# Kernel optimization log

Hardware: AMD Instinct MI355X
Metric: run time of the kernel (lower is better)

## Reference

```python
import jax, jax.numpy as jnp
import numpy as np

B, S, H, R, IN, OPS, NPAD = 128, 128, 512, 16, 2, 5, 16
L = IN + NPAD
NEG = -1e12


def setup_inputs():
    key = jax.random.key(0)
    ks = jax.random.split(key, 32)
    def n(k, shape, scale=1.0):
        return jax.random.normal(k, shape, jnp.float32) * scale
    s = 0.05
    return {
        "encoder_outputs": n(ks[0], (S, B, H)),
        "current_emb": n(ks[1], (B, 1, H)),
        "left_childs": n(ks[2], (B, H)),
        "padding_hidden": jnp.zeros((1, H), jnp.float32),
        "num_pades": n(ks[3], (B, NPAD, H)),
        "rule_scores": n(ks[4], (R, H)),
        "embedding_weight": n(ks[5], (1, IN, H)),
        "W_concat_l": n(ks[6], (H, H), s), "b_concat_l": jnp.zeros((H,)),
        "W_concat_lg": n(ks[7], (H, H), s), "b_concat_lg": jnp.zeros((H,)),
        "W_concat_r": n(ks[8], (2 * H, H), s), "b_concat_r": jnp.zeros((H,)),
        "W_concat_rg": n(ks[9], (2 * H, H), s), "b_concat_rg": jnp.zeros((H,)),
        "W_tree_attn": n(ks[10], (2 * H, H), s), "b_tree_attn": jnp.zeros((H,)),
        "W_tree_score": n(ks[11], (H, 1), s), "b_tree_score": jnp.zeros((1,)),
        "W_rule_attn": n(ks[12], (2 * H, H), s), "b_rule_attn": jnp.zeros((H,)),
        "W_rule_score": n(ks[13], (H, 1), s), "b_rule_score": jnp.zeros((1,)),
        "W_rp1": n(ks[14], (H, H), s), "b_rp1": jnp.zeros((H,)),
        "W_rp2": n(ks[15], (H, 1), s), "b_rp2": jnp.zeros((1,)),
        "W_sc_attn": n(ks[16], (3 * H, H), s), "b_sc_attn": jnp.zeros((H,)),
        "W_sc_score": n(ks[17], (H, 1), s),
        "W_ops": n(ks[18], (2 * H, OPS), s), "b_ops": jnp.zeros((OPS,)),
        "seq_mask": jax.random.randint(ks[19], (B, S), 0, 2).astype(jnp.int32),
        "mask_nums": jax.random.randint(ks[20], (B, L), 0, 2).astype(jnp.int32),
        "has_left": jax.random.randint(ks[21], (B,), 0, 2).astype(jnp.int32),
        "stack_empty": jax.random.randint(ks[22], (B,), 0, 2).astype(jnp.int32),
    }


def reference(encoder_outputs, current_emb, left_childs, padding_hidden, num_pades,
              rule_scores, embedding_weight,
              W_concat_l, b_concat_l, W_concat_lg, b_concat_lg,
              W_concat_r, b_concat_r, W_concat_rg, b_concat_rg,
              W_tree_attn, b_tree_attn, W_tree_score, b_tree_score,
              W_rule_attn, b_rule_attn, W_rule_score, b_rule_score,
              W_rp1, b_rp1, W_rp2, b_rp2,
              W_sc_attn, b_sc_attn, W_sc_score, W_ops, b_ops,
              seq_mask, mask_nums, has_left, stack_empty):
    sm = seq_mask.astype(bool)          # [B,S] True = pad
    nm = mask_nums.astype(bool)         # [B,L]
    hl = has_left.astype(bool)[:, None]
    se = stack_empty.astype(bool)[:, None]
    h = encoder_outputs.shape[-1]
    # gather top-of-stack embedding, padding for empty stacks (the ragged python loop)
    c = jnp.where(se, padding_hidden[0], current_emb[:, 0])  # [B,H]
    # gated combine: left_child==None branch vs cat(left, c) branch (dropout=eval)
    node_l = jnp.tanh(c @ W_concat_l + b_concat_l) * jax.nn.sigmoid(c @ W_concat_lg + b_concat_lg)
    node_r = (jnp.tanh(left_childs @ W_concat_r[:h] + c @ W_concat_r[h:] + b_concat_r)
              * jax.nn.sigmoid(left_childs @ W_concat_rg[:h] + c @ W_concat_rg[h:] + b_concat_rg))
    q = jnp.where(hl, node_r, node_l)                        # [B,H]
    current_node = q[:, None, :]                              # [B,1,H]
    # TreeAttn: concat(hidden, enc) -> Linear -> tanh -> Linear(H,1) -> softmax over S
    e = jnp.tanh(q @ W_tree_attn[:h] + encoder_outputs @ W_tree_attn[h:] + b_tree_attn)  # [S,B,H]
    ae = (e @ W_tree_score)[..., 0] + b_tree_score[0]         # [S,B]
    ae = jnp.where(sm, NEG, ae.T)                             # [B,S]
    current_attn = jax.nn.softmax(ae, axis=1)                 # [B,S]
    current_context = jnp.einsum('bs,sbh->bh', current_attn, encoder_outputs)[:, None, :]
    # RuleAttn: concat(enc, rule) additive attention, softmax over S
    re = jnp.tanh(encoder_outputs @ W_rule_attn[:h]
                  + (rule_scores @ W_rule_attn[h:])[:, None, None, :]
                  + b_rule_attn)                              # [R,S,B,H]
    r_ae = (re @ W_rule_score)[..., 0] + b_rule_score[0]      # [R,S,B]
    r_ae = jnp.transpose(r_ae, (2, 0, 1))                     # [B,R,S]
    r_ae = jnp.where(sm[:, None, :], NEG, r_ae)
    rules_attn = jax.nn.softmax(r_ae, axis=-1)
    rules_context = jnp.einsum('brs,sbh->brh', rules_attn + 0.2 * current_attn[:, None, :], encoder_outputs)
    rule_prob = jax.nn.softmax((jnp.tanh(rules_context @ W_rp1 + b_rp1) @ W_rp2)[..., 0] + b_rp2[0], axis=-1)  # [B,R]
    # leaf scoring: Score(cat(node, context), [const_embs | num_pades])
    bsz = q.shape[0]
    ew = jnp.concatenate([jnp.broadcast_to(embedding_weight, (bsz,) + embedding_weight.shape[1:]), num_pades], axis=1)  # [B,L,H]
    leaf = jnp.concatenate([q, current_context[:, 0]], axis=1)  # [B,2H]
    sc = jnp.tanh((leaf @ W_sc_attn[:2 * h])[:, None, :] + ew @ W_sc_attn[2 * h:] + b_sc_attn)  # [B,L,H]
    num_score = jnp.where(nm, NEG, (sc @ W_sc_score)[..., 0])   # [B,L]
    op = leaf @ W_ops + b_ops                                   # [B,OPS]
    return num_score, op, current_node, current_context, ew, rule_prob
```

## Files before the change

### kernel.cpp

```cpp
#include <hip/hip_runtime.h>
#include <hip/hip_bf16.h>

#define B_ 128
#define S_ 128
#define H_ 512
#define R_ 16
#define IN_ 2
#define OPS_ 5
#define NPAD_ 16
#define L_ 18
#define NEGV (-1000000000000.0f)
#define C2_ (-2.885390081777927f)

typedef __bf16 bf16_t;
typedef bf16_t bf16x8 __attribute__((ext_vector_type(8)));
typedef float floatx4 __attribute__((ext_vector_type(4)));

__device__ __forceinline__ float rcp_f(float x) { return __builtin_amdgcn_rcpf(x); }
__device__ __forceinline__ float exp2_f(float x) { return __builtin_amdgcn_exp2f(x); }

__device__ __forceinline__ float fast_tanh(float x) {
    return 2.0f * rcp_f(1.0f + exp2_f(C2_ * x)) - 1.0f;
}
__device__ __forceinline__ float fast_sigmoid(float x) {
    return rcp_f(1.0f + exp2_f(-1.4426950408889634f * x));
}
__device__ __forceinline__ unsigned short f2bf(float f) {
    unsigned int u = __builtin_bit_cast(unsigned int, f);
    u += 0x7fff + ((u >> 16) & 1);
    return (unsigned short)(u >> 16);
}
__device__ __forceinline__ float bf2f(unsigned short u) {
    return __builtin_bit_cast(float, (unsigned int)u << 16);
}

#define LSTR 40

__device__ __forceinline__ void mfma_tile(const unsigned short* __restrict__ A,
                                          const unsigned short* __restrict__ Bt,
                                          void* __restrict__ Cv, bool bf16_out,
                                          int m0, int n0, int K, int ldc,
                                          unsigned short* As, unsigned short* Bs) {
    const int tid  = threadIdx.x;
    const int wid  = tid >> 6, lane = tid & 63;
    const int quad = lane >> 4, mn = lane & 15;
    const int wm = (wid & 1) * 64, wn = (wid >> 1) * 64;
    const int sr = tid >> 2;
    const int sc = (tid & 3) * 8;

    const unsigned short* pa0 = A  + (size_t)(m0 + sr)      * K + sc;
    const unsigned short* pa1 = A  + (size_t)(m0 + sr + 64) * K + sc;
    const unsigned short* pb0 = Bt + (size_t)(n0 + sr)      * K + sc;
    const unsigned short* pb1 = Bt + (size_t)(n0 + sr + 64) * K + sc;

    uint4 a0 = *(const uint4*)pa0;
    uint4 a1 = *(const uint4*)pa1;
    uint4 b0 = *(const uint4*)pb0;
    uint4 b1 = *(const uint4*)pb1;

    floatx4 acc[4][4] = {};

    for (int k0 = 0; k0 < K; k0 += 32) {
        __syncthreads();
        *(uint4*)&As[sr * LSTR + sc]        = a0;
        *(uint4*)&As[(sr + 64) * LSTR + sc] = a1;
        *(uint4*)&Bs[sr * LSTR + sc]        = b0;
        *(uint4*)&Bs[(sr + 64) * LSTR + sc] = b1;
        __syncthreads();

        if (k0 + 32 < K) {
            a0 = *(const uint4*)(pa0 + k0 + 32);
            a1 = *(const uint4*)(pa1 + k0 + 32);
            b0 = *(const uint4*)(pb0 + k0 + 32);
            b1 = *(const uint4*)(pb1 + k0 + 32);
        }

        bf16x8 af[4], bfr[4];
        #pragma unroll
        for (int i = 0; i < 4; ++i)
            af[i] = *(const bf16x8*)&As[(wm + i * 16 + mn) * LSTR + quad * 8];
        #pragma unroll
        for (int j = 0; j < 4; ++j)
            bfr[j] = *(const bf16x8*)&Bs[(wn + j * 16 + mn) * LSTR + quad * 8];

        #pragma unroll
        for (int i = 0; i < 4; ++i)
            #pragma unroll
            for (int j = 0; j < 4; ++j)
                acc[i][j] = __builtin_amdgcn_mfma_f32_16x16x32_bf16(af[i], bfr[j], acc[i][j], 0, 0, 0);
    }

    #pragma unroll
    for (int i = 0; i < 4; ++i) {
        #pragma unroll
        for (int j = 0; j < 4; ++j) {
            #pragma unroll
            for (int r = 0; r < 4; ++r) {
                int row = m0 + wm + i * 16 + quad * 4 + r;
                int col = n0 + wn + j * 16 + mn;
                if (bf16_out)
                    ((unsigned short*)Cv)[(size_t)row * ldc + col] = f2bf(acc[i][j][r]);
                else
                    ((float*)Cv)[(size_t)row * ldc + col] = acc[i][j][r];
            }
        }
    }
}

__global__ __launch_bounds__(256) void k_gemm_mega1(const unsigned short* __restrict__ EO_bf,
                                                    const unsigned short* __restrict__ Wcat,
                                                    unsigned short* __restrict__ eobuf,
                                                    const unsigned short* __restrict__ q_bf,
                                                    const unsigned short* __restrict__ T5,
                                                    float* __restrict__ qT) {
    __shared__ unsigned short As[128 * LSTR];
    __shared__ unsigned short Bs[128 * LSTR];
    int blk = blockIdx.x;
    if (blk < 1024)
        mfma_tile(EO_bf, Wcat, eobuf, true, (blk & 127) * 128, (blk >> 7) * 128, 512, 1024, As, Bs);
    else
        mfma_tile(q_bf, T5, qT, false, 0, (blk - 1024) * 128, 512, 512, As, Bs);
}

__global__ __launch_bounds__(256) void k_gemm_mega2(const unsigned short* __restrict__ rctx_bf,
                                                    const unsigned short* __restrict__ T8,
                                                    float* __restrict__ rclin,
                                                    const unsigned short* __restrict__ leaf_bf,
                                                    const unsigned short* __restrict__ T9,
                                                    float* __restrict__ lsb,
                                                    const unsigned short* __restrict__ ew_bf,
                                                    const unsigned short* __restrict__ T10,
                                                    unsigned short* __restrict__ ewp_bf) {
    __shared__ unsigned short As[128 * LSTR];
    __shared__ unsigned short Bs[128 * LSTR];
    int blk = blockIdx.x;
    if (blk < 64)
        mfma_tile(rctx_bf, T8, rclin, false, (blk >> 2) * 128, (blk & 3) * 128, 512, 512, As, Bs);
    else if (blk < 68)
        mfma_tile(leaf_bf, T9, lsb, false, 0, (blk - 64) * 128, 1024, 512, As, Bs);
    else {
        int r = blk - 68;
        mfma_tile(ew_bf, T10, ewp_bf, true, (r >> 2) * 128, (r & 3) * 128, 512, 512, As, Bs);
    }
}

struct MJ5 {
    const unsigned short* A[5]; const unsigned short* Bt[5]; float* C[5];
    int M[5]; int K[5];
};
__global__ __launch_bounds__(256) void gemm_bf16_j5(MJ5 g) {
    __shared__ unsigned short As[128 * LSTR];
    __shared__ unsigned short Bs[128 * LSTR];

    const int z = blockIdx.z;
    const unsigned short* A  = g.A[z];
    const unsigned short* Bt = g.Bt[z];
    float* C = g.C[z];
    const int M = g.M[z], K = g.K[z];

    const int tid  = threadIdx.x;
    const int wid  = tid >> 6, lane = tid & 63;
    const int quad = lane >> 4, mn = lane & 15;
    const int wm = (wid & 1) * 64, wn = (wid >> 1) * 64;
    const int n0 = blockIdx.x * 128;

    const int sr = tid >> 2;
    const int sc = (tid & 3) * 8;
    const int ra0 = min(sr, M - 1);
    const int ra1 = min(sr + 64, M - 1);

    const unsigned short* pa0 = A  + (size_t)ra0 * K + sc;
    const unsigned short* pa1 = A  + (size_t)ra1 * K + sc;
    const unsigned short* pb0 = Bt + (size_t)(n0 + sr)      * K + sc;
    const unsigned short* pb1 = Bt + (size_t)(n0 + sr + 64) * K + sc;

    uint4 a0 = *(const uint4*)pa0;
    uint4 a1 = *(const uint4*)pa1;
    uint4 b0 = *(const uint4*)pb0;
    uint4 b1 = *(const uint4*)pb1;

    floatx4 acc[4][4] = {};

    for (int k0 = 0; k0 < K; k0 += 32) {
        __syncthreads();
        *(uint4*)&As[sr * LSTR + sc]        = a0;
        *(uint4*)&As[(sr + 64) * LSTR + sc] = a1;
        *(uint4*)&Bs[sr * LSTR + sc]        = b0;
        *(uint4*)&Bs[(sr + 64) * LSTR + sc] = b1;
        __syncthreads();

        if (k0 + 32 < K) {
            a0 = *(const uint4*)(pa0 + k0 + 32);
            a1 = *(const uint4*)(pa1 + k0 + 32);
            b0 = *(const uint4*)(pb0 + k0 + 32);
            b1 = *(const uint4*)(pb1 + k0 + 32);
        }

        bf16x8 af[4], bfr[4];
        #pragma unroll
        for (int i = 0; i < 4; ++i)
            af[i] = *(const bf16x8*)&As[(wm + i * 16 + mn) * LSTR + quad * 8];
        #pragma unroll
        for (int j = 0; j < 4; ++j)
            bfr[j] = *(const bf16x8*)&Bs[(wn + j * 16 + mn) * LSTR + quad * 8];

        #pragma unroll
        for (int i = 0; i < 4; ++i)
            #pragma unroll
            for (int j = 0; j < 4; ++j)
                acc[i][j] = __builtin_amdgcn_mfma_f32_16x16x32_bf16(af[i], bfr[j], acc[i][j], 0, 0, 0);
    }

    #pragma unroll
    for (int i = 0; i < 4; ++i) {
        #pragma unroll
        for (int j = 0; j < 4; ++j) {
            #pragma unroll
            for (int r = 0; r < 4; ++r) {
                int row = wm + i * 16 + quad * 4 + r;
                int col = n0 + wn + j * 16 + mn;
                if (row < M)
                    C[(size_t)row * 512 + col] = acc[i][j][r];
            }
        }
    }
}

struct PrepArgs {
    const float *EO, *cur, *padh, *left, *rsc, *embw, *npad;
    const int* se;
    unsigned short *EO_bf, *c_bf, *acat_bf, *rsc_bf, *ew_bf;
    float* ew_out;
    const float* tsrc[11];
    unsigned short* tdst[11];
    int tK[11];
    int tbase[12];
};
#define PG_CAST 8192
#define PG_EW   1152
#define PG_PREP 288
#define PG_WT   3584
#define PG_TOTAL (PG_CAST + PG_EW + PG_PREP + PG_WT)

__global__ __launch_bounds__(256) void k_prep_mega(PrepArgs a) {
    __shared__ float t[32][33];
    int blk = blockIdx.x, tid = threadIdx.x;
    if (blk < PG_CAST) {
        int i = (blk * 256 + tid) * 4;
        float4 v = *(const float4*)(a.EO + i);
        ushort4 o;
        o.x = f2bf(v.x); o.y = f2bf(v.y); o.z = f2bf(v.z); o.w = f2bf(v.w);
        *(ushort4*)(a.EO_bf + i) = o;
    } else if (blk < PG_CAST + PG_EW) {
        int i = ((blk - PG_CAST) * 256 + tid) * 4;
        int j = i & 511;
        int bl = i >> 9;
        int l = bl % L_;
        int b = bl / L_;
        const float* src = (l < IN_) ? (a.embw + l * H_ + j)
                                     : (a.npad + ((size_t)b * NPAD_ + (l - IN_)) * H_ + j);
        float4 v = *(const float4*)src;
        *(float4*)(a.ew_out + i) = v;
        ushort4 o;
        o.x = f2bf(v.x); o.y = f2bf(v.y); o.z = f2bf(v.z); o.w = f2bf(v.w);
        *(ushort4*)(a.ew_bf + i) = o;
    } else if (blk < PG_CAST + PG_EW + PG_PREP) {
        int i = (blk - PG_CAST - PG_EW) * 256 + tid;
        if (i < B_ * H_) {
            int b = i >> 9, j = i & 511;
            float cv = a.se[b] ? a.padh[j] : a.cur[i];
            a.c_bf[i] = f2bf(cv);
            a.acat_bf[b * 1024 + j] = f2bf(a.left[i]);
            a.acat_bf[b * 1024 + 512 + j] = f2bf(cv);
        } else {
            int k = i - B_ * H_;
            a.rsc_bf[k] = f2bf(a.rsc[k]);
        }
    } else {
        int rel = blk - (PG_CAST + PG_EW + PG_PREP);
        int j = 0;
        while (rel >= a.tbase[j + 1]) ++j;
        int r = rel - a.tbase[j];
        int K = a.tK[j];
        const float* src = a.tsrc[j];
        unsigned short* dst = a.tdst[j];
        int bx = (r & 15) * 32;
        int by = (r >> 4) * 32;
        int tx = tid & 31, ty = tid >> 5;
        #pragma unroll
        for (int i = 0; i < 32; i += 8)
            t[ty + i][tx] = src[(size_t)(by + ty + i) * 512 + bx + tx];
        __syncthreads();
        #pragma unroll
        for (int i = 0; i < 32; i += 8)
            dst[(size_t)(bx + ty + i) * K + by + tx] = f2bf(t[tx][ty + i]);
    }
}

__global__ void k_node(const float* __restrict__ gl, const float* __restrict__ glg,
                       const float* __restrict__ gr, const float* __restrict__ grg,
                       const float* __restrict__ bl, const float* __restrict__ blg,
                       const float* __restrict__ br, const float* __restrict__ brg,
                       const int* __restrict__ hl,
                       unsigned short* __restrict__ q_bf, float* __restrict__ node_out,
                       unsigned short* __restrict__ leaf_bf) {
    int i = blockIdx.x * blockDim.x + threadIdx.x;
    int b = i >> 9, j = i & 511;
    float nl = fast_tanh(gl[i] + bl[j]) * fast_sigmoid(glg[i] + blg[j]);
    float nr = fast_tanh(gr[i] + br[j]) * fast_sigmoid(grg[i] + brg[j]);
    float v = hl[b] ? nr : nl;
    node_out[i] = v;
    q_bf[i] = f2bf(v);
    leaf_bf[b * 1024 + j] = f2bf(v);
}

__global__ __launch_bounds__(256) void k_score_fused(const float* __restrict__ qT,
                                                     const unsigned short* __restrict__ eobuf,
                                                     const float* __restrict__ b_ta,
                                                     const float* __restrict__ w_ts,
                                                     const float* __restrict__ b_ts,
                                                     const float* __restrict__ RP,
                                                     const float* __restrict__ b_ra,
                                                     const float* __restrict__ w_rs,
                                                     const float* __restrict__ b_rs,
                                                     const int* __restrict__ sm,
                                                     float* __restrict__ attn,
                                                     float* __restrict__ comb) {
    __shared__ float sc[S_];
    int blk = blockIdx.x;
    int tid = threadIdx.x;
    int wid = tid >> 6, lane = tid & 63;
    int j0 = lane * 8;

    if (blk < 128) {
        int b = blk;
        float4 q0 = *(const float4*)(qT + b * H_ + j0);
        float4 q1 = *(const float4*)(qT + b * H_ + j0 + 4);
        float4 t0 = *(const float4*)(b_ta + j0);
        float4 t1 = *(const float4*)(b_ta + j0 + 4);
        float4 w0 = *(const float4*)(w_ts + j0);
        float4 w1 = *(const float4*)(w_ts + j0 + 4);
        float qc[8] = {C2_*(q0.x+t0.x), C2_*(q0.y+t0.y), C2_*(q0.z+t0.z), C2_*(q0.w+t0.w),
                       C2_*(q1.x+t1.x), C2_*(q1.y+t1.y), C2_*(q1.z+t1.z), C2_*(q1.w+t1.w)};
        float w2[8] = {2*w0.x, 2*w0.y, 2*w0.z, 2*w0.w, 2*w1.x, 2*w1.y, 2*w1.z, 2*w1.w};
        float wsum = 0.5f * (w2[0]+w2[1]+w2[2]+w2[3]+w2[4]+w2[5]+w2[6]+w2[7]);
        float bias = b_ts[0];

        for (int s = wid; s < S_; s += 4) {
            if (sm[b * S_ + s]) {
                if (lane == 0) sc[s] = NEGV;
                continue;
            }
            uint4 ev = *(const uint4*)(eobuf + ((size_t)s * B_ + b) * 1024 + j0);
            const unsigned short* ep = (const unsigned short*)&ev;
            float acc = -wsum;
            #pragma unroll
            for (int k = 0; k < 8; ++k) {
                float y = fmaf(C2_, bf2f(ep[k]), qc[k]);
                acc = fmaf(w2[k], rcp_f(1.0f + exp2_f(y)), acc);
            }
            #pragma unroll
            for (int o = 32; o > 0; o >>= 1) acc += __shfl_xor(acc, o);
            if (lane == 0) sc[s] = acc + bias;
        }
        __syncthreads();
        if (tid < 64) {
            float v0 = sc[tid], v1 = sc[tid + 64];
            float m = fmaxf(v0, v1);
            #pragma unroll
            for (int o = 32; o > 0; o >>= 1) m = fmaxf(m, __shfl_xor(m, o));
            float e0 = __expf(v0 - m), e1 = __expf(v1 - m);
            float ss = e0 + e1;
            #pragma unroll
            for (int o = 32; o > 0; o >>= 1) ss += __shfl_xor(ss, o);
            float r = rcp_f(ss);
            attn[b * S_ + tid] = e0 * r;
            attn[b * S_ + tid + 64] = e1 * r;
        }
        return;
    }

    int row = (blk - 128) * 4 + wid;
    int s = row >> 7, b = row & 127;
    bool masked = sm[b * S_ + s] != 0;
    if (masked) {
        if (lane < R_) comb[((size_t)b * R_ + lane) * S_ + s] = NEGV;
        return;
    }
    uint4 ev = *(const uint4*)(eobuf + (size_t)row * 1024 + 512 + j0);
    const unsigned short* ep = (const unsigned short*)&ev;
    float4 a0 = *(const float4*)(b_ra + j0);
    float4 a1 = *(const float4*)(b_ra + j0 + 4);
    float4 w0 = *(const float4*)(w_rs + j0);
    float4 w1 = *(const float4*)(w_rs + j0 + 4);
    float ba[8] = {a0.x, a0.y, a0.z, a0.w, a1.x, a1.y, a1.z, a1.w};
    float w2[8], ed[8];
    float wsum = 0.f;
    {
        float w[8] = {w0.x, w0.y, w0.z, w0.w, w1.x, w1.y, w1.z, w1.w};
        #pragma unroll
        for (int k = 0; k < 8; ++k) {
            wsum += w[k];
            w2[k] = 2.0f * w[k];
            ed[k] = C2_ * (bf2f(ep[k]) + ba[k]);
        }
    }
    float bias = b_rs[0];
    #pragma unroll
    for (int r = 0; r < R_; ++r) {
        float4 r0 = *(const float4*)(RP + r * H_ + j0);
        float4 r1 = *(const float4*)(RP + r * H_ + j0 + 4);
        float rp[8] = {r0.x, r0.y, r0.z, r0.w, r1.x, r1.y, r1.z, r1.w};
        float acc = -wsum;
        #pragma unroll
        for (int k = 0; k < 8; ++k) {
            float y = fmaf(C2_, rp[k], ed[k]);
            acc = fmaf(w2[k], rcp_f(1.0f + exp2_f(y)), acc);
        }
        #pragma unroll
        for (int o = 32; o > 0; o >>= 1) acc += __shfl_xor(acc, o);
        if (lane == 0) comb[((size_t)b * R_ + r) * S_ + s] = acc + bias;
    }
}

__global__ __launch_bounds__(512) void k_ctxsm(const unsigned short* __restrict__ EO_bf,
                                               const float* __restrict__ attn,
                                               const float* __restrict__ comb,
                                               const int* __restrict__ sm,
                                               float* __restrict__ ctx_out,
                                               unsigned short* __restrict__ leaf_bf,
                                               unsigned short* __restrict__ rctx) {
    __shared__ float cb[R_ * S_];
    __shared__ float at[S_];
    __shared__ int smr[S_];
    int b = blockIdx.x;
    int tid = threadIdx.x;
    int w = tid >> 6, lane = tid & 63;

    if (tid < S_) {
        at[tid] = attn[b * S_ + tid];
        smr[tid] = sm[b * S_ + tid];
    }
    for (int i = tid; i < R_ * S_; i += 512) cb[i] = comb[(size_t)b * R_ * S_ + i];
    __syncthreads();

    #pragma unroll
    for (int rr = 0; rr < 2; ++rr) {
        int r = w * 2 + rr;
        float v0 = cb[r * S_ + lane], v1 = cb[r * S_ + lane + 64];
        float m = fmaxf(v0, v1);
        #pragma unroll
        for (int o = 32; o > 0; o >>= 1) m = fmaxf(m, __shfl_xor(m, o));
        float e0 = __expf(v0 - m), e1 = __expf(v1 - m);
        float ss = e0 + e1;
        #pragma unroll
        for (int o = 32; o > 0; o >>= 1) ss += __shfl_xor(ss, o);
        float rc_ = rcp_f(ss);
        cb[r * S_ + lane]      = e0 * rc_ + 0.2f * at[lane];
        cb[r * S_ + lane + 64] = e1 * rc_ + 0.2f * at[lane + 64];
    }
    __syncthreads();

    int j = tid;
    float ctx = 0.f;
    float rc[R_] = {};
    for (int s = 0; s < S_; ++s) {
        if (smr[s]) continue;
        float eo = bf2f(EO_bf[((size_t)s * B_ + b) * H_ + j]);
        ctx += at[s] * eo;
        #pragma unroll
        for (int r = 0; r < R_; ++r) rc[r] += cb[r * S_ + s] * eo;
    }
    ctx_out[b * H_ + j] = ctx;
    leaf_bf[b * 1024 + 512 + j] = f2bf(ctx);
    #pragma unroll
    for (int r = 0; r < R_; ++r) rctx[((size_t)b * R_ + r) * H_ + j] = f2bf(rc[r]);
}

__global__ __launch_bounds__(256) void k_epilogue(const float* __restrict__ rclin,
                                                  const float* __restrict__ b_rp1,
                                                  const float* __restrict__ w_rp2,
                                                  const float* __restrict__ b_rp2,
                                                  float* __restrict__ prob,
                                                  const float* __restrict__ lsb,
                                                  const unsigned short* __restrict__ ewp,
                                                  const float* __restrict__ b_sc,
                                                  const float* __restrict__ w_scs,
                                                  const int* __restrict__ mask_nums,
                                                  float* __restrict__ ns_out,
                                                  const unsigned short* __restrict__ leaf_bf,
                                                  const float* __restrict__ Wops,
                                                  const float* __restrict__ bops,
                                                  float* __restrict__ op_out) {
    __shared__ float sc[R_];
    int blk = blockIdx.x;
    int wid = threadIdx.x >> 6, lane = threadIdx.x & 63;
    if (blk < 128) {
        int b = blk;
        int j0 = lane * 8;
        float4 p0 = *(const float4*)(b_rp1 + j0);
        float4 p1 = *(const float4*)(b_rp1 + j0 + 4);
        float4 w0 = *(const float4*)(w_rp2 + j0);
        float4 w1 = *(const float4*)(w_rp2 + j0 + 4);
        float brc[8] = {C2_*p0.x, C2_*p0.y, C2_*p0.z, C2_*p0.w,
                        C2_*p1.x, C2_*p1.y, C2_*p1.z, C2_*p1.w};
        float w[8] = {w0.x, w0.y, w0.z, w0.w, w1.x, w1.y, w1.z, w1.w};
        float wsum = 0.f;
        #pragma unroll
        for (int k = 0; k < 8; ++k) wsum += w[k];
        #pragma unroll
        for (int rr = 0; rr < 4; ++rr) {
            int r = wid * 4 + rr;
            const float* rl = rclin + ((size_t)b * R_ + r) * H_ + j0;
            float4 r0 = *(const float4*)(rl);
            float4 r1 = *(const float4*)(rl + 4);
            float rv[8] = {r0.x, r0.y, r0.z, r0.w, r1.x, r1.y, r1.z, r1.w};
            float acc = -wsum;
            #pragma unroll
            for (int k = 0; k < 8; ++k) {
                float y = fmaf(C2_, rv[k], brc[k]);
                acc = fmaf(2.0f * w[k], rcp_f(1.0f + exp2_f(y)), acc);
            }
            #pragma unroll
            for (int o = 32; o > 0; o >>= 1) acc += __shfl_xor(acc, o);
            if (lane == 0) sc[r] = acc + b_rp2[0];
        }
        __syncthreads();
        if (threadIdx.x < R_) {
            float m = -1e30f;
            for (int r = 0; r < R_; ++r) m = fmaxf(m, sc[r]);
            float sum = 0.f;
            for (int r = 0; r < R_; ++r) sum += __expf(sc[r] - m);
            prob[b * R_ + threadIdx.x] = __expf(sc[threadIdx.x] - m) * rcp_f(sum);
        }
    } else if (blk < 704) {
        int row = (blk - 128) * 4 + wid;
        int b = row / L_, l = row - b * L_;
        bool masked = mask_nums[b * L_ + l] != 0;
        if (masked) {
            if (lane == 0) ns_out[b * L_ + l] = NEGV;
            return;
        }
        int j0 = lane * 8;
        uint4 ev = *(const uint4*)(ewp + (size_t)row * H_ + j0);
        const unsigned short* ep = (const unsigned short*)&ev;
        float4 l0 = *(const float4*)(lsb + b * H_ + j0);
        float4 l1 = *(const float4*)(lsb + b * H_ + j0 + 4);
        float4 s0 = *(const float4*)(b_sc + j0);
        float4 s1 = *(const float4*)(b_sc + j0 + 4);
        float4 w0 = *(const float4*)(w_scs + j0);
        float4 w1 = *(const float4*)(w_scs + j0 + 4);
        float lc[8] = {C2_*(l0.x+s0.x), C2_*(l0.y+s0.y), C2_*(l0.z+s0.z), C2_*(l0.w+s0.w),
                       C2_*(l1.x+s1.x), C2_*(l1.y+s1.y), C2_*(l1.z+s1.z), C2_*(l1.w+s1.w)};
        float w[8] = {w0.x, w0.y, w0.z, w0.w, w1.x, w1.y, w1.z, w1.w};
        float wsum = 0.f;
        #pragma unroll
        for (int k = 0; k < 8; ++k) wsum += w[k];
        float acc = -wsum;
        #pragma unroll
        for (int k = 0; k < 8; ++k) {
            float y = fmaf(C2_, bf2f(ep[k]), lc[k]);
            acc = fmaf(2.0f * w[k], rcp_f(1.0f + exp2_f(y)), acc);
        }
        #pragma unroll
        for (int o = 32; o > 0; o >>= 1) acc += __shfl_xor(acc, o);
        if (lane == 0) ns_out[b * L_ + l] = acc;
    } else {
        int b = (blk - 704) * 4 + wid;
        int base = b * 1024 + lane * 16;
        uint4 v0 = *(const uint4*)(leaf_bf + base);
        uint4 v1 = *(const uint4*)(leaf_bf + base + 8);
        const unsigned short* lp0 = (const unsigned short*)&v0;
        const unsigned short* lp1 = (const unsigned short*)&v1;
        float lv[16];
        #pragma unroll
        for (int k = 0; k < 8; ++k) { lv[k] = bf2f(lp0[k]); lv[8 + k] = bf2f(lp1[k]); }
        #pragma unroll
        for (int o = 0; o < OPS_; ++o) {
            float acc = 0.f;
            #pragma unroll
            for (int k = 0; k < 16; ++k)
                acc = fmaf(lv[k], Wops[(size_t)(lane * 16 + k) * OPS_ + o], acc);
            #pragma unroll
            for (int of = 32; of > 0; of >>= 1) acc += __shfl_xor(acc, of);
            if (lane == 0) op_out[b * OPS_ + o] = acc + bops[o];
        }
    }
}

extern "C" void kernel_launch(void* const* d_in, const int* in_sizes, int n_in,
                              void* d_out, int out_size, void* d_ws, size_t ws_size,
                              hipStream_t stream) {
    const float* EO   = (const float*)d_in[0];
    const float* cur  = (const float*)d_in[1];
    const float* left = (const float*)d_in[2];
    const float* padh = (const float*)d_in[3];
    const float* npad = (const float*)d_in[4];
    const float* rsc  = (const float*)d_in[5];
    const float* embw = (const float*)d_in[6];
    const float* Wl   = (const float*)d_in[7];  const float* bl   = (const float*)d_in[8];
    const float* Wlg  = (const float*)d_in[9];  const float* blg  = (const float*)d_in[10];
    const float* Wr   = (const float*)d_in[11]; const float* br   = (const float*)d_in[12];
    const float* Wrg  = (const float*)d_in[13]; const float* brg  = (const float*)d_in[14];
    const float* Wta  = (const float*)d_in[15]; const float* bta  = (const float*)d_in[16];
    const float* Wts  = (const float*)d_in[17]; const float* bts  = (const float*)d_in[18];
    const float* Wra  = (const float*)d_in[19]; const float* bra  = (const float*)d_in[20];
    const float* Wrs  = (const float*)d_in[21]; const float* brs  = (const float*)d_in[22];
    const float* Wrp1 = (const float*)d_in[23]; const float* brp1 = (const float*)d_in[24];
    const float* Wrp2 = (const float*)d_in[25]; const float* brp2 = (const float*)d_in[26];
    const float* Wsa  = (const float*)d_in[27]; const float* bsa  = (const float*)d_in[28];
    const float* Wss  = (const float*)d_in[29];
    const float* Wops = (const float*)d_in[30]; const float* bops = (const float*)d_in[31];
    const int* smk = (const int*)d_in[32];
    const int* nmk = (const int*)d_in[33];
    const int* hlk = (const int*)d_in[34];
    const int* sek = (const int*)d_in[35];

    float* out = (float*)d_out;

    const size_t O_NS    = 0;
    const size_t O_OP    = O_NS + (size_t)B_ * L_;
    const size_t O_NODE  = O_OP + (size_t)B_ * OPS_;
    const size_t O_CTX   = O_NODE + (size_t)B_ * H_;
    const size_t O_EW    = O_CTX + (size_t)B_ * H_;
    const size_t O_RPROB = O_EW + (size_t)B_ * L_ * H_;

    float* f = (float*)d_ws;
    float* rp_buf = f;               f += 8192;
    float* qT     = f;               f += 65536;
    float* attn   = f;               f += 16384;
    float* comb   = f;               f += 262144;
    float* gl     = f;               f += 65536;
    float* glg    = f;               f += 65536;
    float* gr     = f;               f += 65536;
    float* grg    = f;               f += 65536;
    float* lsb    = f;               f += 65536;
    float* rclin  = f;               f += 1048576;
    unsigned short* u = (unsigned short*)f;
    unsigned short* EO_bf   = u;     u += 8388608;
    unsigned short* ew_bf   = u;     u += 1179648;
    unsigned short* leaf_bf = u;     u += 131072;
    unsigned short* rctx_bf = u;     u += 1048576;
    unsigned short* Wcat    = u;     u += 524288;
    unsigned short* T0      = u;     u += 262144;
    unsigned short* T1      = u;     u += 262144;
    unsigned short* T2      = u;     u += 524288;
    unsigned short* T3      = u;     u += 524288;
    unsigned short* T4      = u;     u += 262144;
    unsigned short* T5      = u;     u += 262144;
    unsigned short* T8      = u;     u += 262144;
    unsigned short* T9      = u;     u += 524288;
    unsigned short* T10     = u;     u += 262144;
    unsigned short* q_bf    = u;     u += 65536;
    unsigned short* c_bf    = u;     u += 65536;
    unsigned short* acat_bf = u;     u += 131072;
    unsigned short* rsc_bf  = u;     u += 8192;
    unsigned short* ewp_bf  = u;     u += 1179648;
    unsigned short* eobuf   = u;     u += 16777216;

    PrepArgs a;
    a.EO = EO; a.cur = cur; a.padh = padh; a.left = left; a.rsc = rsc;
    a.embw = embw; a.npad = npad; a.se = sek;
    a.EO_bf = EO_bf; a.c_bf = c_bf; a.acat_bf = acat_bf; a.rsc_bf = rsc_bf;
    a.ew_bf = ew_bf; a.ew_out = out + O_EW;
    const float* tsrc[11] = {Wl, Wlg, Wr, Wrg, Wra + (size_t)H_ * H_, Wta,
                             Wta + (size_t)H_ * H_, Wra, Wrp1, Wsa, Wsa + (size_t)2 * H_ * H_};
    unsigned short* tdst[11] = {T0, T1, T2, T3, T4, T5, Wcat, Wcat + 512 * 512, T8, T9, T10};
    int tk[11] = {512, 512, 1024, 1024, 512, 512, 512, 512, 512, 1024, 512};
    int base = 0;
    for (int i = 0; i < 11; ++i) {
        a.tsrc[i] = tsrc[i]; a.tdst[i] = tdst[i]; a.tK[i] = tk[i];
        a.tbase[i] = base;
        base += 16 * (tk[i] / 32);
    }
    a.tbase[11] = base;
    k_prep_mega<<<PG_TOTAL, 256, 0, stream>>>(a);

    MJ5 g;
    g.A[0] = c_bf;    g.Bt[0] = T0; g.C[0] = gl;     g.M[0] = B_;  g.K[0] = 512;
    g.A[1] = c_bf;    g.Bt[1] = T1; g.C[1] = glg;    g.M[1] = B_;  g.K[1] = 512;
    g.A[2] = acat_bf; g.Bt[2] = T2; g.C[2] = gr;     g.M[2] = B_;  g.K[2] = 1024;
    g.A[3] = acat_bf; g.Bt[3] = T3; g.C[3] = grg;    g.M[3] = B_;  g.K[3] = 1024;
    g.A[4] = rsc_bf;  g.Bt[4] = T4; g.C[4] = rp_buf; g.M[4] = R_;  g.K[4] = 512;
    gemm_bf16_j5<<<dim3(4, 1, 5), 256, 0, stream>>>(g);

    k_node<<<256, 256, 0, stream>>>(gl, glg, gr, grg, bl, blg, br, brg, hlk,
                                    q_bf, out + O_NODE, leaf_bf);

    k_gemm_mega1<<<1028, 256, 0, stream>>>(EO_bf, Wcat, eobuf, q_bf, T5, qT);

    k_score_fused<<<128 + S_ * B_ / 4, 256, 0, stream>>>(
        qT, eobuf, bta, Wts, bts, rp_buf, bra, Wrs, brs, smk, attn, comb);

    k_ctxsm<<<B_, 512, 0, stream>>>(EO_bf, attn, comb, smk, out + O_CTX,
                                    leaf_bf, rctx_bf);

    k_gemm_mega2<<<140, 256, 0, stream>>>(rctx_bf, T8, rclin, leaf_bf, T9, lsb,
                                          ew_bf, T10, ewp_bf);

    k_epilogue<<<736, 256, 0, stream>>>(rclin, brp1, Wrp2, brp2, out + O_RPROB,
                                        lsb, ewp_bf, bsa, Wss, nmk, out + O_NS,
                                        leaf_bf, Wops, bops, out + O_OP);
}
```

Before: 298.2 us.

## Double-buffer GEMM LDS tiles, vectorize epilogue stores, split ctx kernel over H

The shared GEMM tile routines now use two LDS buffers, so the next K-slice is written while MFMAs consume the current one, cutting one barrier per iteration. MFMA operands are swapped so each lane holds four consecutive output columns, which lets the epilogue write float4/ushort4 vectors instead of scalar stores. The context kernel is split into two 256-thread blocks per batch row along H and walks a compacted list of unmasked positions instead of branching on the mask. This doubles LDS per GEMM block, which may lower occupancy, and builds the position list serially in one thread.

```diff
diff --git a/kernel.cpp b/kernel.cpp
--- a/kernel.cpp
+++ b/kernel.cpp
@@ -35,6 +35,7 @@
 }
 
 #define LSTR 40
+#define LBUF (128 * LSTR)
 
 __device__ __forceinline__ void mfma_tile(const unsigned short* __restrict__ A,
                                           const unsigned short* __restrict__ Bt,
@@ -57,51 +58,69 @@
     uint4 a1 = *(const uint4*)pa1;
     uint4 b0 = *(const uint4*)pb0;
     uint4 b1 = *(const uint4*)pb1;
+    *(uint4*)&As[sr * LSTR + sc]        = a0;
+    *(uint4*)&As[(sr + 64) * LSTR + sc] = a1;
+    *(uint4*)&Bs[sr * LSTR + sc]        = b0;
+    *(uint4*)&Bs[(sr + 64) * LSTR + sc] = b1;
+    if (K > 32) {
+        a0 = *(const uint4*)(pa0 + 32);
+        a1 = *(const uint4*)(pa1 + 32);
+        b0 = *(const uint4*)(pb0 + 32);
+        b1 = *(const uint4*)(pb1 + 32);
+    }
+    __syncthreads();
 
     floatx4 acc[4][4] = {};
 
     for (int k0 = 0; k0 < K; k0 += 32) {
-        __syncthreads();
-        *(uint4*)&As[sr * LSTR + sc]        = a0;
-        *(uint4*)&As[(sr + 64) * LSTR + sc] = a1;
-        *(uint4*)&Bs[sr * LSTR + sc]        = b0;
-        *(uint4*)&Bs[(sr + 64) * LSTR + sc] = b1;
-        __syncthreads();
+        const int cur = (k0 >> 5) & 1;
+        unsigned short* Asb = As + cur * LBUF;
+        unsigned short* Bsb = Bs + cur * LBUF;
+
+        bf16x8 af[4], bfr[4];
+        #pragma unroll
+        for (int i = 0; i < 4; ++i)
+            af[i] = *(const bf16x8*)&Asb[(wm + i * 16 + mn) * LSTR + quad * 8];
+        #pragma unroll
+        for (int j = 0; j < 4; ++j)
+            bfr[j] = *(const bf16x8*)&Bsb[(wn + j * 16 + mn) * LSTR + quad * 8];
+
+        #pragma unroll
+        for (int i = 0; i < 4; ++i)
+            #pragma unroll
+            for (int j = 0; j < 4; ++j)
+                acc[i][j] = __builtin_amdgcn_mfma_f32_16x16x32_bf16(bfr[j], af[i], acc[i][j], 0, 0, 0);
 
         if (k0 + 32 < K) {
-            a0 = *(const uint4*)(pa0 + k0 + 32);
-            a1 = *(const uint4*)(pa1 + k0 + 32);
-            b0 = *(const uint4*)(pb0 + k0 + 32);
-            b1 = *(const uint4*)(pb1 + k0 + 32);
-        }
-
-        bf16x8 af[4], bfr[4];
-        #pragma unroll
-        for (int i = 0; i < 4; ++i)
-            af[i] = *(const bf16x8*)&As[(wm + i * 16 + mn) * LSTR + quad * 8];
-        #pragma unroll
-        for (int j = 0; j < 4; ++j)
-            bfr[j] = *(const bf16x8*)&Bs[(wn + j * 16 + mn) * LSTR + quad * 8];
-
-        #pragma unroll
-        for (int i = 0; i < 4; ++i)
-            #pragma unroll
-            for (int j = 0; j < 4; ++j)
-                acc[i][j] = __builtin_amdgcn_mfma_f32_16x16x32_bf16(af[i], bfr[j], acc[i][j], 0, 0, 0);
+            unsigned short* Asn = As + (cur ^ 1) * LBUF;
+            unsigned short* Bsn = Bs + (cur ^ 1) * LBUF;
+            *(uint4*)&Asn[sr * LSTR + sc]        = a0;
+            *(uint4*)&Asn[(sr + 64) * LSTR + sc] = a1;
+            *(uint4*)&Bsn[sr * LSTR + sc]        = b0;
+            *(uint4*)&Bsn[(sr + 64) * LSTR + sc] = b1;
+            if (k0 + 64 < K) {
+                a0 = *(const uint4*)(pa0 + k0 + 64);
+                a1 = *(const uint4*)(pa1 + k0 + 64);
+                b0 = *(const uint4*)(pb0 + k0 + 64);
+                b1 = *(const uint4*)(pb1 + k0 + 64);
+            }
+            __syncthreads();
+        }
     }
 
     #pragma unroll
     for (int i = 0; i < 4; ++i) {
+        int row = m0 + wm + i * 16 + mn;
         #pragma unroll
         for (int j = 0; j < 4; ++j) {
-            #pragma unroll
-            for (int r = 0; r < 4; ++r) {
-                int row = m0 + wm + i * 16 + quad * 4 + r;
-                int col = n0 + wn + j * 16 + mn;
-                if (bf16_out)
-                    ((unsigned short*)Cv)[(size_t)row * ldc + col] = f2bf(acc[i][j][r]);
-                else
-                    ((float*)Cv)[(size_t)row * ldc + col] = acc[i][j][r];
+            int col = n0 + wn + j * 16 + quad * 4;
+            if (bf16_out) {
+                ushort4 v = {f2bf(acc[i][j][0]), f2bf(acc[i][j][1]),
+                             f2bf(acc[i][j][2]), f2bf(acc[i][j][3])};
+                *(ushort4*)((unsigned short*)Cv + (size_t)row * ldc + col) = v;
+            } else {
+                float4 v = {acc[i][j][0], acc[i][j][1], acc[i][j][2], acc[i][j][3]};
+                *(float4*)((float*)Cv + (size_t)row * ldc + col) = v;
             }
         }
     }
@@ -113,8 +132,8 @@
                                                     const unsigned short* __restrict__ q_bf,
                                                     const unsigned short* __restrict__ T5,
                                                     float* __restrict__ qT) {
-    __shared__ unsigned short As[128 * LSTR];
-    __shared__ unsigned short Bs[128 * LSTR];
+    __shared__ unsigned short As[2 * LBUF];
+    __shared__ unsigned short Bs[2 * LBUF];
     int blk = blockIdx.x;
     if (blk < 1024)
         mfma_tile(EO_bf, Wcat, eobuf, true, (blk & 127) * 128, (blk >> 7) * 128, 512, 1024, As, Bs);
@@ -131,8 +150,8 @@
                                                     const unsigned short* __restrict__ ew_bf,
                                                     const unsigned short* __restrict__ T10,
                                                     unsigned short* __restrict__ ewp_bf) {
-    __shared__ unsigned short As[128 * LSTR];
-    __shared__ unsigned short Bs[128 * LSTR];
+    __shared__ unsigned short As[2 * LBUF];
+    __shared__ unsigned short Bs[2 * LBUF];
     int blk = blockIdx.x;
     if (blk < 64)
         mfma_tile(rctx_bf, T8, rclin, false, (blk >> 2) * 128, (blk & 3) * 128, 512, 512, As, Bs);
@@ -149,8 +168,8 @@
     int M[5]; int K[5];
 };
 __global__ __launch_bounds__(256) void gemm_bf16_j5(MJ5 g) {
-    __shared__ unsigned short As[128 * LSTR];
-    __shared__ unsigned short Bs[128 * LSTR];
+    __shared__ unsigned short As[2 * LBUF];
+    __shared__ unsigned short Bs[2 * LBUF];
 
     const int z = blockIdx.z;
     const unsigned short* A  = g.A[z];
@@ -178,49 +197,65 @@
     uint4 a1 = *(const uint4*)pa1;
     uint4 b0 = *(const uint4*)pb0;
     uint4 b1 = *(const uint4*)pb1;
+    *(uint4*)&As[sr * LSTR + sc]        = a0;
+    *(uint4*)&As[(sr + 64) * LSTR + sc] = a1;
+    *(uint4*)&Bs[sr * LSTR + sc]        = b0;
+    *(uint4*)&Bs[(sr + 64) * LSTR + sc] = b1;
+    if (K > 32) {
+        a0 = *(const uint4*)(pa0 + 32);
+        a1 = *(const uint4*)(pa1 + 32);
+        b0 = *(const uint4*)(pb0 + 32);
+        b1 = *(const uint4*)(pb1 + 32);
+    }
+    __syncthreads();
 
     floatx4 acc[4][4] = {};
 
     for (int k0 = 0; k0 < K; k0 += 32) {
-        __syncthreads();
-        *(uint4*)&As[sr * LSTR + sc]        = a0;
-        *(uint4*)&As[(sr + 64) * LSTR + sc] = a1;
-        *(uint4*)&Bs[sr * LSTR + sc]        = b0;
-        *(uint4*)&Bs[(sr + 64) * LSTR + sc] = b1;
-        __syncthreads();
+        const int cur = (k0 >> 5) & 1;
+        unsigned short* Asb = As + cur * LBUF;
+        unsigned short* Bsb = Bs + cur * LBUF;
+
+        bf16x8 af[4], bfr[4];
+        #pragma unroll
+        for (int i = 0; i < 4; ++i)
+            af[i] = *(const bf16x8*)&Asb[(wm + i * 16 + mn) * LSTR + quad * 8];
+        #pragma unroll
+        for (int j = 0; j < 4; ++j)
+            bfr[j] = *(const bf16x8*)&Bsb[(wn + j * 16 + mn) * LSTR + quad * 8];
+
+        #pragma unroll
+        for (int i = 0; i < 4; ++i)
+            #pragma unroll
+            for (int j = 0; j < 4; ++j)
+                acc[i][j] = __builtin_amdgcn_mfma_f32_16x16x32_bf16(bfr[j], af[i], acc[i][j], 0, 0, 0);
 
         if (k0 + 32 < K) {
-            a0 = *(const uint4*)(pa0 + k0 + 32);
-            a1 = *(const uint4*)(pa1 + k0 + 32);
-            b0 = *(const uint4*)(pb0 + k0 + 32);
-            b1 = *(const uint4*)(pb1 + k0 + 32);
-        }
-
-        bf16x8 af[4], bfr[4];
-        #pragma unroll
-        for (int i = 0; i < 4; ++i)
-            af[i] = *(const bf16x8*)&As[(wm + i * 16 + mn) * LSTR + quad * 8];
-        #pragma unroll
-        for (int j = 0; j < 4; ++j)
-            bfr[j] = *(const bf16x8*)&Bs[(wn + j * 16 + mn) * LSTR + quad * 8];
-
-        #pragma unroll
-        for (int i = 0; i < 4; ++i)
-            #pragma unroll
-            for (int j = 0; j < 4; ++j)
-                acc[i][j] = __builtin_amdgcn_mfma_f32_16x16x32_bf16(af[i], bfr[j], acc[i][j], 0, 0, 0);
+            unsigned short* Asn = As + (cur ^ 1) * LBUF;
+            unsigned short* Bsn = Bs + (cur ^ 1) * LBUF;
+            *(uint4*)&Asn[sr * LSTR + sc]        = a0;
+            *(uint4*)&Asn[(sr + 64) * LSTR + sc] = a1;
+            *(uint4*)&Bsn[sr * LSTR + sc]        = b0;
+            *(uint4*)&Bsn[(sr + 64) * LSTR + sc] = b1;
+            if (k0 + 64 < K) {
+                a0 = *(const uint4*)(pa0 + k0 + 64);
+                a1 = *(const uint4*)(pa1 + k0 + 64);
+                b0 = *(const uint4*)(pb0 + k0 + 64);
+                b1 = *(const uint4*)(pb1 + k0 + 64);
+            }
+            __syncthreads();
+        }
     }
 
     #pragma unroll
     for (int i = 0; i < 4; ++i) {
-        #pragma unroll
-        for (int j = 0; j < 4; ++j) {
-            #pragma unroll
-            for (int r = 0; r < 4; ++r) {
-                int row = wm + i * 16 + quad * 4 + r;
-                int col = n0 + wn + j * 16 + mn;
-                if (row < M)
-                    C[(size_t)row * 512 + col] = acc[i][j][r];
+        int row = wm + i * 16 + mn;
+        if (row < M) {
+            #pragma unroll
+            for (int j = 0; j < 4; ++j) {
+                int col = n0 + wn + j * 16 + quad * 4;
+                float4 v = {acc[i][j][0], acc[i][j][1], acc[i][j][2], acc[i][j][3]};
+                *(float4*)(C + (size_t)row * 512 + col) = v;
             }
         }
     }
@@ -423,7 +458,7 @@
     }
 }
 
-__global__ __launch_bounds__(512) void k_ctxsm(const unsigned short* __restrict__ EO_bf,
+__global__ __launch_bounds__(256) void k_ctxsm(const unsigned short* __restrict__ EO_bf,
                                                const float* __restrict__ attn,
                                                const float* __restrict__ comb,
                                                const int* __restrict__ sm,
@@ -432,21 +467,25 @@
                                                unsigned short* __restrict__ rctx) {
     __shared__ float cb[R_ * S_];
     __shared__ float at[S_];
-    __shared__ int smr[S_];
+    __shared__ short usl[S_];
+    __shared__ int ucount;
     int b = blockIdx.x;
     int tid = threadIdx.x;
     int w = tid >> 6, lane = tid & 63;
 
-    if (tid < S_) {
-        at[tid] = attn[b * S_ + tid];
-        smr[tid] = sm[b * S_ + tid];
-    }
-    for (int i = tid; i < R_ * S_; i += 512) cb[i] = comb[(size_t)b * R_ * S_ + i];
+    if (tid < S_) at[tid] = attn[b * S_ + tid];
+    for (int i = tid; i < R_ * S_; i += 256) cb[i] = comb[(size_t)b * R_ * S_ + i];
+    if (tid == 0) {
+        int c = 0;
+        for (int s = 0; s < S_; ++s)
+            if (!sm[b * S_ + s]) usl[c++] = (short)s;
+        ucount = c;
+    }
     __syncthreads();
 
     #pragma unroll
-    for (int rr = 0; rr < 2; ++rr) {
-        int r = w * 2 + rr;
+    for (int rr = 0; rr < 4; ++rr) {
+        int r = w * 4 + rr;
         float v0 = cb[r * S_ + lane], v1 = cb[r * S_ + lane + 64];
         float m = fmaxf(v0, v1);
         #pragma unroll
@@ -461,11 +500,13 @@
     }
     __syncthreads();
 
-    int j = tid;
+    int j = blockIdx.y * 256 + tid;
+    int nu = ucount;
     float ctx = 0.f;
     float rc[R_] = {};
-    for (int s = 0; s < S_; ++s) {
-        if (smr[s]) continue;
+    #pragma unroll 2
+    for (int ii = 0; ii < nu; ++ii) {
+        int s = usl[ii];
         float eo = bf2f(EO_bf[((size_t)s * B_ + b) * H_ + j]);
         ctx += at[s] * eo;
         #pragma unroll
@@ -692,8 +733,8 @@
     k_score_fused<<<128 + S_ * B_ / 4, 256, 0, stream>>>(
         qT, eobuf, bta, Wts, bts, rp_buf, bra, Wrs, brs, smk, attn, comb);
 
-    k_ctxsm<<<B_, 512, 0, stream>>>(EO_bf, attn, comb, smk, out + O_CTX,
-                                    leaf_bf, rctx_bf);
+    k_ctxsm<<<dim3(B_, 2), 256, 0, stream>>>(EO_bf, attn, comb, smk, out + O_CTX,
+                                             leaf_bf, rctx_bf);
 
     k_gemm_mega2<<<140, 256, 0, stream>>>(rctx_bf, T8, rclin, leaf_bf, T9, lsb,
                                           ew_bf, T10, ewp_bf);
```

New measurement: 284.7 us. -4.5%, faster.
